# Kernel tuning notes

Measured on AMD Instinct MI355X. Metric: run time of the kernel, lower is better.

The kernel has to match this reference:

```python
import jax, jax.numpy as jnp
import numpy as np

TAU = 0.1          # contrastive_temperature
EPS = 0.05         # property_epsilon
L_LOCAL_G, L_GLOBAL, L_SC_G, L_LOCAL_SC, G_PROP = 1.0, 0.8, 1.0, 0.8, 0.5
B = 4096
D = 256
NUM_PROPS = 4
N_ATOMS = 131072
N_MOTIFS = 32768


def setup_inputs() -> dict:
    key = jax.random.key(0)
    ks = jax.random.split(key, 10)
    return {
        "emb_g_mole": jax.random.normal(ks[0], (B, D), jnp.float32),
        "emb_g_frag": jax.random.normal(ks[1], (N_ATOMS, D), jnp.float32),
        "emb_sc_mole": jax.random.normal(ks[2], (B, D), jnp.float32),
        "emb_sc_shape": jax.random.normal(ks[3], (N_MOTIFS, D), jnp.float32),
        "emb_motif": jax.random.normal(ks[4], (N_MOTIFS, D), jnp.float32),
        "emb_shape": jax.random.normal(ks[5], (N_MOTIFS, D), jnp.float32),
        # scaled so duplicate rows are the only pairs within EPS (realistic sparse mask)
        "prop_pred": jax.random.normal(ks[6], (B, NUM_PROPS), jnp.float32) * 0.05,
        "prop_target": jax.random.normal(ks[7], (B, NUM_PROPS), jnp.float32) * 0.05,
        "batch_g": jax.random.randint(ks[8], (N_ATOMS,), 0, B, jnp.int32),
        "batch_sc": jax.random.randint(ks[9], (N_MOTIFS,), 0, B, jnp.int32),
    }


def _contrastive(emb, props):
    # SupervisedContrastiveLoss: normalized cosine logits, mask from sqrt(cdist) < eps
    n = emb.shape[0]
    e = emb / jnp.maximum(jnp.linalg.norm(emb, axis=1, keepdims=True), 1e-12)
    logits = jnp.matmul(e, e.T) / TAU                       # [n, n]
    log_probs = jax.nn.log_softmax(logits, axis=1)
    sq = jnp.sum(props * props, axis=1)
    d2 = jnp.maximum(sq[:, None] + sq[None, :] - 2.0 * jnp.matmul(props, props.T), 0.0)
    dd = jnp.sqrt(jnp.sqrt(d2)) + 1e-8                      # cdist(...).sqrt() + 1e-8
    mask = (dd < EPS) & (~jnp.eye(n, dtype=bool))           # fill_diagonal_(0)
    cnt = jnp.sum(mask, axis=1)
    row_loss = -jnp.sum(jnp.where(mask, log_probs, 0.0), axis=1) / jnp.maximum(cnt, 1)
    valid = cnt > 0
    nvalid = jnp.sum(valid)
    loss = jnp.sum(jnp.where(valid, row_loss, 0.0)) / jnp.maximum(nvalid, 1)
    return jnp.where(nvalid > 0, loss, 0.0)


def _frag_alignment(emb_g_frag, emb_motif, batch_g, batch_sc):
    ones_g = jnp.ones((emb_g_frag.shape[0],), emb_g_frag.dtype)
    ones_s = jnp.ones((emb_motif.shape[0],), emb_motif.dtype)
    cnt_g = jax.ops.segment_sum(ones_g, batch_g, num_segments=B)
    cnt_s = jax.ops.segment_sum(ones_s, batch_sc, num_segments=B)
    mean_g = jax.ops.segment_sum(emb_g_frag, batch_g, num_segments=B) / jnp.maximum(cnt_g, 1.0)[:, None]
    mean_s = jax.ops.segment_sum(emb_motif, batch_sc, num_segments=B) / jnp.maximum(cnt_s, 1.0)[:, None]
    norms = jnp.linalg.norm(mean_g - mean_s, axis=1)
    valid = (cnt_g > 0) & (cnt_s > 0)
    batch_size = batch_g.max().astype(emb_g_frag.dtype) + 1.0
    return jnp.sum(jnp.where(valid, norms, 0.0)) / batch_size


def reference(emb_g_mole, emb_g_frag, emb_sc_mole, emb_sc_shape, emb_motif,
              emb_shape, prop_pred, prop_target, batch_g, batch_sc):
    l_local_g = _frag_alignment(emb_g_frag, emb_motif, batch_g, batch_sc)
    combined_emb = jnp.concatenate([emb_g_mole, emb_sc_mole], axis=0)    # [2B, d]
    combined_props = jnp.concatenate([prop_pred, prop_pred], axis=0)      # [2B, p]
    l_contr = _contrastive(combined_emb, combined_props)
    l_global = l_contr          # same inputs in both calls -> identical value
    l_local_sc = l_contr
    l_sc_g = jnp.mean(jnp.linalg.norm(emb_sc_shape - emb_shape, axis=1))  # AlignmentLoss mean
    l_prop = jnp.mean((prop_pred - prop_target) ** 2)                     # MSELoss
    l_hes = (L_LOCAL_G * l_local_g + L_GLOBAL * l_global + L_SC_G * l_sc_g
             + L_LOCAL_SC * l_local_sc + G_PROP * l_prop)
    # stacked: [l_hes, l_local_g, l_global, l_sc_g, l_local_sc, l_prop]
    return jnp.stack([l_hes, l_local_g, l_global, l_sc_g, l_local_sc, l_prop])
```

## Files before the change

kernel.cpp:

```cpp
#include <hip/hip_runtime.h>
#include <hip/hip_bf16.h>
#include <stdint.h>

typedef unsigned short u16;
typedef float f32x4 __attribute__((ext_vector_type(4)));
typedef short s16x8 __attribute__((ext_vector_type(8)));
typedef u16   u16x8 __attribute__((ext_vector_type(8)));
typedef u16   u16x4 __attribute__((ext_vector_type(4)));
typedef uint32_t u32x4 __attribute__((ext_vector_type(4)));

#define B_      4096
#define D_      256
#define NA_     131072
#define NM_     32768
#define N2_     8192
#define THR4    6.2499950e-6f
#define K2E     14.426950408889634f

#define OFF_CNT_G   0u
#define OFF_CNT_S   16384u
#define OFF_CUR_G   32768u
#define OFF_CUR_S   49152u
#define OFF_NB      65536u
#define OFF_SCAL    81920u
#define OFF_S       98304u
#define ZERO_BYTES  131072u
#define OFF_T       131072u
#define OFF_C       163840u
#define OFF_PLIST   196608u
#define OFF_OFFS_G  720896u
#define OFF_OFFS_S  737280u
#define OFF_SORT_G  753664u
#define OFF_SORT_S  1277952u
#define OFF_E       1409024u
#define WS_NEED     5603328u

__device__ inline float wave_sum(float v) {
#pragma unroll
  for (int m = 1; m < 64; m <<= 1) v += __shfl_xor(v, m, 64);
  return v;
}
__device__ inline int wave_sum_i(int v) {
#pragma unroll
  for (int m = 1; m < 64; m <<= 1) v += __shfl_xor(v, m, 64);
  return v;
}
__device__ inline u16 f2bf(float f) {
  uint32_t u = __float_as_uint(f);
  uint32_t r = (u + 0x7FFFu + ((u >> 16) & 1u)) >> 16;
  return (u16)r;
}
__device__ inline float bf2f(u16 v) { return __uint_as_float(((uint32_t)v) << 16); }

__device__ inline void gload16(const u16* __restrict__ g, u16* l) {
  __builtin_amdgcn_global_load_lds(
      (const __attribute__((address_space(1))) uint32_t*)g,
      (__attribute__((address_space(3))) uint32_t*)l, 16, 0, 0);
}

__global__ void k_zero(u32x4* __restrict__ p) {
  u32x4 z = {0u, 0u, 0u, 0u};
  p[blockIdx.x * 256 + threadIdx.x] = z;
}

__global__ void k_count(const int* __restrict__ bg, const int* __restrict__ bs,
                        int* cntg, int* cnts, int* bmax) {
  int i = blockIdx.x * 256 + threadIdx.x;
  int b = -1;
  if (i < NA_) { b = bg[i]; atomicAdd(&cntg[b], 1); }
  if (i < NM_) { atomicAdd(&cnts[bs[i]], 1); }
  int m = b;
#pragma unroll
  for (int k = 1; k < 64; k <<= 1) m = max(m, __shfl_xor(m, k, 64));
  if ((threadIdx.x & 63) == 0 && m >= 0) atomicMax(bmax, m);
}

__global__ void k_scan(const int* __restrict__ cntg, const int* __restrict__ cnts,
                       int* offsg, int* offss, int* curg, int* curs) {
  const int* cnt = blockIdx.x == 0 ? cntg : cnts;
  int* offs = blockIdx.x == 0 ? offsg : offss;
  int* cur  = blockIdx.x == 0 ? curg  : curs;
  __shared__ int ls[256];
  int t = threadIdx.x;
  int v[16]; int s = 0;
#pragma unroll
  for (int k = 0; k < 16; k++) { v[k] = cnt[t * 16 + k]; s += v[k]; }
  ls[t] = s;
  __syncthreads();
  for (int off = 1; off < 256; off <<= 1) {
    int add = (t >= off) ? ls[t - off] : 0;
    __syncthreads();
    ls[t] += add;
    __syncthreads();
  }
  int pre = t ? ls[t - 1] : 0;
#pragma unroll
  for (int k = 0; k < 16; k++) { offs[t * 16 + k] = pre; cur[t * 16 + k] = pre; pre += v[k]; }
}

__device__ inline void wave_row_sum(const float* __restrict__ src,
                                    const int* __restrict__ sorted,
                                    int off, int cnt, int lane, f32x4* accs) {
  f32x4 a0 = {0.f,0.f,0.f,0.f}, a1 = a0, a2 = a0, a3 = a0;
  f32x4 a4 = a0, a5 = a0, a6 = a0, a7 = a0;
  for (int base = 0; base < cnt; base += 64) {
    int n = min(cnt - base, 64);
    int idx = (lane < n) ? sorted[off + base + lane] : 0;
    int k = 0;
    for (; k + 7 < n; k += 8) {
      int i0 = __shfl(idx, k,     64), i1 = __shfl(idx, k + 1, 64);
      int i2 = __shfl(idx, k + 2, 64), i3 = __shfl(idx, k + 3, 64);
      int i4 = __shfl(idx, k + 4, 64), i5 = __shfl(idx, k + 5, 64);
      int i6 = __shfl(idx, k + 6, 64), i7 = __shfl(idx, k + 7, 64);
      a0 += *(const f32x4*)(src + (size_t)i0 * D_ + lane * 4);
      a1 += *(const f32x4*)(src + (size_t)i1 * D_ + lane * 4);
      a2 += *(const f32x4*)(src + (size_t)i2 * D_ + lane * 4);
      a3 += *(const f32x4*)(src + (size_t)i3 * D_ + lane * 4);
      a4 += *(const f32x4*)(src + (size_t)i4 * D_ + lane * 4);
      a5 += *(const f32x4*)(src + (size_t)i5 * D_ + lane * 4);
      a6 += *(const f32x4*)(src + (size_t)i6 * D_ + lane * 4);
      a7 += *(const f32x4*)(src + (size_t)i7 * D_ + lane * 4);
    }
    for (; k < n; k++) {
      int i0 = __shfl(idx, k, 64);
      a0 += *(const f32x4*)(src + (size_t)i0 * D_ + lane * 4);
    }
  }
  *accs = ((a0 + a1) + (a2 + a3)) + ((a4 + a5) + (a6 + a7));
}

__global__ __launch_bounds__(256) void k_fuseA(
    const int* __restrict__ bg, const int* __restrict__ bs,
    int* __restrict__ curg, int* __restrict__ curs,
    int* __restrict__ sortg, int* __restrict__ sorts,
    const float* __restrict__ gm, const float* __restrict__ scm,
    const float* __restrict__ scs, const float* __restrict__ shp,
    const float* __restrict__ pp,
    u16* __restrict__ E, int* __restrict__ nb, int* __restrict__ plist,
    float* __restrict__ scal) {
  int t = threadIdx.x, w = t >> 6, lane = t & 63;
  int blk = blockIdx.x;

  if (blk < 4096) {
    int a = blk;
    f32x4 pa = *(const f32x4*)(pp + (size_t)a * 4);
    for (int b = t; b < B_; b += 256) {
      f32x4 pb = *(const f32x4*)(pp + (size_t)b * 4);
      float dx = pa.x - pb.x, dy = pa.y - pb.y, dz = pa.z - pb.z, dw = pa.w - pb.w;
      float d2 = dx * dx + dy * dy + dz * dz + dw * dw;
      if (d2 < THR4) {
        int pos = atomicAdd(&nb[a], 1);
        if (pos < 32) plist[a * 32 + pos] = b;
      }
    }
  } else if (blk < 4608) {
    int i = (blk - 4096) * 256 + t;
    if (i < NA_) { int b = bg[i]; sortg[atomicAdd(&curg[b], 1)] = i; }
    if (i < NM_) { int b = bs[i]; sorts[atomicAdd(&curs[b], 1)] = i; }
  } else if (blk < 6656) {
    int r = (blk - 4608) * 4 + w;
    const float* src = (r < B_) ? gm + (size_t)r * D_ : scm + (size_t)(r - B_) * D_;
    f32x4 v = *(const f32x4*)(src + lane * 4);
    float ss = v.x * v.x + v.y * v.y + v.z * v.z + v.w * v.w;
    ss = wave_sum(ss);
    float inv = 1.f / fmaxf(sqrtf(ss), 1e-12f);
    u16x4 o;
    o.x = f2bf(v.x * inv); o.y = f2bf(v.y * inv);
    o.z = f2bf(v.z * inv); o.w = f2bf(v.w * inv);
    *(u16x4*)(E + (size_t)r * D_ + lane * 4) = o;
  } else {
    int wg = (blk - 6656) * 4 + w;
    float acc = 0.f;
    for (int r = wg; r < NM_; r += 8192) {
      f32x4 va = *(const f32x4*)(scs + (size_t)r * D_ + lane * 4);
      f32x4 vb = *(const f32x4*)(shp + (size_t)r * D_ + lane * 4);
      float dx = va.x - vb.x, dy = va.y - vb.y, dz = va.z - vb.z, dw = va.w - vb.w;
      float ss = wave_sum(dx * dx + dy * dy + dz * dz + dw * dw);
      if (lane == 0) acc += sqrtf(ss);
    }
    __shared__ float sr4[4];
    if (lane == 0) sr4[w] = acc;
    __syncthreads();
    if (t == 0) atomicAdd(&scal[1], sr4[0] + sr4[1] + sr4[2] + sr4[3]);
  }
}

__global__ __launch_bounds__(256) void k_fuseB(
    const u16* __restrict__ E,
    const float* __restrict__ fg, const float* __restrict__ fm,
    const int* __restrict__ cntg, const int* __restrict__ cnts,
    const int* __restrict__ offsg, const int* __restrict__ offss,
    const int* __restrict__ sortg, const int* __restrict__ sorts,
    const int* __restrict__ nb, const int* __restrict__ plist,
    float* __restrict__ S, float* __restrict__ T, int* __restrict__ C,
    float* __restrict__ scal) {
  __shared__ __align__(16) u16 As[128 * 64];
  __shared__ __align__(16) u16 Bs[128 * 64];
  int blk = blockIdx.x;
  int tid = threadIdx.x, lane = tid & 63, wid = tid >> 6;

  if (blk < 1024) {
    int b = blk * 4 + wid;
    int cg = cntg[b], cs = cnts[b];
    int og = offsg[b], os = offss[b];
    f32x4 sg, ss;
    wave_row_sum(fg, sortg, og, cg, lane, &sg);
    wave_row_sum(fm, sorts, os, cs, lane, &ss);
    float ig = 1.f / fmaxf((float)cg, 1.f);
    float is = 1.f / fmaxf((float)cs, 1.f);
    float dx = sg.x * ig - ss.x * is, dy = sg.y * ig - ss.y * is;
    float dz = sg.z * ig - ss.z * is, dw = sg.w * ig - ss.w * is;
    float v = wave_sum(dx * dx + dy * dy + dz * dz + dw * dw);
    __shared__ float r2[4];
    if (lane == 0) r2[wid] = (cg > 0 && cs > 0) ? sqrtf(v) : 0.f;
    __syncthreads();
    if (tid == 0) {
      float s = r2[0] + r2[1] + r2[2] + r2[3];
      if (s != 0.f) atomicAdd(&scal[0], s);
    }
    return;
  }

  if (blk >= 3104) {
    int i = (blk - 3104) * 4 + wid;
    int a = i & (B_ - 1);
    int n = min(nb[a], 32);
    u16x4 vi = *(const u16x4*)(E + (size_t)i * D_ + lane * 4);
    float ex = bf2f(vi.x), ey = bf2f(vi.y), ez = bf2f(vi.z), ew = bf2f(vi.w);
    float acc = -(ex * ex + ey * ey + ez * ez + ew * ew);
    for (int k = 0; k < n; k++) {
      int b = plist[a * 32 + k];
      u16x4 v1 = *(const u16x4*)(E + (size_t)b * D_ + lane * 4);
      u16x4 v2 = *(const u16x4*)(E + (size_t)(b + B_) * D_ + lane * 4);
      acc += ex * bf2f(v1.x) + ey * bf2f(v1.y) + ez * bf2f(v1.z) + ew * bf2f(v1.w);
      acc += ex * bf2f(v2.x) + ey * bf2f(v2.y) + ez * bf2f(v2.z) + ew * bf2f(v2.w);
    }
    acc = wave_sum(acc);
    if (lane == 0) { T[i] = 10.0f * acc; C[i] = 2 * n - 1; }
    return;
  }

  int t = blk - 1024;
  int bi = (int)((129.0f - sqrtf(129.0f * 129.0f - 8.0f * (float)t)) * 0.5f);
  while ((bi + 1) * (129 - (bi + 1)) / 2 <= t) bi++;
  while (bi * (129 - bi) / 2 > t) bi--;
  int bj = bi + (t - bi * (129 - bi) / 2);

  int row0 = bi * 128, col0 = bj * 128;
  int wr = wid >> 1, wc = wid & 1;

  int rsub = lane >> 3;
  int csw  = (((lane & 7) ^ rsub) << 4) >> 1;

  f32x4 acc[4][4];
#pragma unroll
  for (int mi = 0; mi < 4; mi++)
#pragma unroll
    for (int ni = 0; ni < 4; ni++) {
      f32x4 z = {0.f, 0.f, 0.f, 0.f};
      acc[mi][ni] = z;
    }

  for (int kc = 0; kc < 4; ++kc) {
    __syncthreads();
#pragma unroll
    for (int it = 0; it < 4; it++) {
      int s = wid * 4 + it;
      int r = s * 8 + rsub;
      gload16(E + (size_t)(row0 + r) * D_ + kc * 64 + csw, As + s * 512);
      gload16(E + (size_t)(col0 + r) * D_ + kc * 64 + csw, Bs + s * 512);
    }
    __syncthreads();
#pragma unroll
    for (int kk = 0; kk < 2; ++kk) {
      s16x8 af[4], bfr[4];
#pragma unroll
      for (int mi = 0; mi < 4; mi++) {
        int rA = wr * 64 + mi * 16 + (lane & 15);
        int cbf = kk * 64 + (lane >> 4) * 16;
        int addr = rA * 128 + (cbf ^ ((rA & 7) << 4));
        af[mi] = *(const s16x8*)((const char*)As + addr);
      }
#pragma unroll
      for (int ni = 0; ni < 4; ni++) {
        int rB = wc * 64 + ni * 16 + (lane & 15);
        int cbf = kk * 64 + (lane >> 4) * 16;
        int addr = rB * 128 + (cbf ^ ((rB & 7) << 4));
        bfr[ni] = *(const s16x8*)((const char*)Bs + addr);
      }
#pragma unroll
      for (int mi = 0; mi < 4; mi++)
#pragma unroll
        for (int ni = 0; ni < 4; ni++)
          acc[mi][ni] = __builtin_amdgcn_mfma_f32_16x16x32_bf16(af[mi], bfr[ni], acc[mi][ni], 0, 0, 0);
    }
  }

  int g = lane >> 4, cl = lane & 15;
  float colsum[4] = {0.f, 0.f, 0.f, 0.f};
#pragma unroll
  for (int mi = 0; mi < 4; mi++) {
#pragma unroll
    for (int reg = 0; reg < 4; ++reg) {
      int gi = row0 + wr * 64 + mi * 16 + g * 4 + reg;
      float vs = 0.f;
#pragma unroll
      for (int ni = 0; ni < 4; ni++) {
        float e = exp2f(acc[mi][ni][reg] * K2E - K2E);
        vs += e;
        colsum[ni] += e;
      }
#pragma unroll
      for (int m = 1; m < 16; m <<= 1) vs += __shfl_xor(vs, m, 64);
      if (cl == 0) atomicAdd(&S[gi], vs);
    }
  }
  if (bi != bj) {
#pragma unroll
    for (int ni = 0; ni < 4; ni++) {
      float cs = colsum[ni];
      cs += __shfl_xor(cs, 16, 64);
      cs += __shfl_xor(cs, 32, 64);
      if (g == 0) atomicAdd(&S[col0 + wc * 64 + ni * 16 + cl], cs);
    }
  }
}

__global__ void k_final(const float* __restrict__ S, const float* __restrict__ T,
                        const int* __restrict__ C, const float* __restrict__ scal,
                        const float* __restrict__ pp, const float* __restrict__ pt,
                        float* __restrict__ out) {
  float sp = 0.f;
  for (int i = threadIdx.x; i < B_ * 4; i += 256) {
    float d = pp[i] - pt[i];
    sp += d * d;
  }
  float rls = 0.f; int nv = 0;
  for (int i = threadIdx.x; i < N2_; i += 256) {
    int ci = C[i];
    if (ci > 0) { rls += (10.0f + logf(S[i])) - T[i] / (float)ci; nv++; }
  }
  rls = wave_sum(rls);
  sp  = wave_sum(sp);
  nv  = wave_sum_i(nv);
  __shared__ float r1[4], r3[4]; __shared__ int r2[4];
  int lane = threadIdx.x & 63, w = threadIdx.x >> 6;
  if (lane == 0) { r1[w] = rls; r2[w] = nv; r3[w] = sp; }
  __syncthreads();
  if (threadIdx.x == 0) {
    float rtot = r1[0] + r1[1] + r1[2] + r1[3];
    int nvt = r2[0] + r2[1] + r2[2] + r2[3];
    float sptot = r3[0] + r3[1] + r3[2] + r3[3];
    float l_contr = nvt > 0 ? rtot / (float)nvt : 0.f;
    int bmax = ((const int*)scal)[3];
    float bs = (float)bmax + 1.0f;
    float l_local_g = scal[0] / bs;
    float l_sc = scal[1] / (float)NM_;
    float l_prop = sptot / (float)(B_ * 4);
    float l_hes = 1.0f * l_local_g + 0.8f * l_contr + 1.0f * l_sc + 0.8f * l_contr + 0.5f * l_prop;
    out[0] = l_hes; out[1] = l_local_g; out[2] = l_contr;
    out[3] = l_sc;  out[4] = l_contr;   out[5] = l_prop;
  }
}

extern "C" void kernel_launch(void* const* d_in, const int* in_sizes, int n_in,
                              void* d_out, int out_size, void* d_ws, size_t ws_size,
                              hipStream_t stream) {
  if (ws_size < WS_NEED) return;
  const float* gm  = (const float*)d_in[0];
  const float* fg  = (const float*)d_in[1];
  const float* scm = (const float*)d_in[2];
  const float* scs = (const float*)d_in[3];
  const float* mot = (const float*)d_in[4];
  const float* shp = (const float*)d_in[5];
  const float* pp  = (const float*)d_in[6];
  const float* pt  = (const float*)d_in[7];
  const int* bg = (const int*)d_in[8];
  const int* bs = (const int*)d_in[9];
  float* out = (float*)d_out;
  char* ws = (char*)d_ws;

  int* cntg  = (int*)(ws + OFF_CNT_G);
  int* cnts  = (int*)(ws + OFF_CNT_S);
  int* curg  = (int*)(ws + OFF_CUR_G);
  int* curs  = (int*)(ws + OFF_CUR_S);
  int* nb    = (int*)(ws + OFF_NB);
  float* scal = (float*)(ws + OFF_SCAL);
  float* S   = (float*)(ws + OFF_S);
  float* T   = (float*)(ws + OFF_T);
  int* C     = (int*)(ws + OFF_C);
  int* plist = (int*)(ws + OFF_PLIST);
  int* offsg = (int*)(ws + OFF_OFFS_G);
  int* offss = (int*)(ws + OFF_OFFS_S);
  int* sortg = (int*)(ws + OFF_SORT_G);
  int* sorts = (int*)(ws + OFF_SORT_S);
  u16* E     = (u16*)(ws + OFF_E);

  k_zero<<<32, 256, 0, stream>>>((u32x4*)ws);
  k_count<<<512, 256, 0, stream>>>(bg, bs, cntg, cnts, (int*)scal + 3);
  k_scan<<<2, 256, 0, stream>>>(cntg, cnts, offsg, offss, curg, curs);
  k_fuseA<<<8704, 256, 0, stream>>>(bg, bs, curg, curs, sortg, sorts,
                                    gm, scm, scs, shp, pp, E, nb, plist, scal);
  k_fuseB<<<5152, 256, 0, stream>>>(E, fg, mot, cntg, cnts, offsg, offss,
                                    sortg, sorts, nb, plist, S, T, C, scal);
  k_final<<<1, 256, 0, stream>>>(S, T, C, scal, pp, pt, out);
}
```

Baseline: 213.4 us.

## Restructure stage fusion and interleave segment, GEMM and diag blocks in fuseB

Moves the histogram count into the fused elementwise kernel and splits the scatter into its own small kernel after the scan. In k_fuseB, segment-sum, GEMM-tile and diagonal-term blocks are interleaved by a proportional index mapping instead of being laid out in contiguous ranges. The diagonal-term blocks now each handle 32 rows, cutting the grid from 5152 to 3360 blocks. The aim is to balance memory-bound and compute-bound blocks across the GPU and shorten tail effects, at the cost of an extra kernel launch and more index arithmetic.

```diff
diff --git a/kernel.cpp b/kernel.cpp
--- a/kernel.cpp
+++ b/kernel.cpp
@@ -16,6 +16,12 @@
 #define N2_     8192
 #define THR4    6.2499950e-6f
 #define K2E     14.426950408889634f
+
+#define NS_   1024
+#define NG_   2080
+#define NT_   256
+#define NTOT_ 3360
+#define NR_   2336
 
 #define OFF_CNT_G   0u
 #define OFF_CNT_S   16384u
@@ -63,16 +69,64 @@
   p[blockIdx.x * 256 + threadIdx.x] = z;
 }
 
-__global__ void k_count(const int* __restrict__ bg, const int* __restrict__ bs,
-                        int* cntg, int* cnts, int* bmax) {
-  int i = blockIdx.x * 256 + threadIdx.x;
-  int b = -1;
-  if (i < NA_) { b = bg[i]; atomicAdd(&cntg[b], 1); }
-  if (i < NM_) { atomicAdd(&cnts[bs[i]], 1); }
-  int m = b;
-#pragma unroll
-  for (int k = 1; k < 64; k <<= 1) m = max(m, __shfl_xor(m, k, 64));
-  if ((threadIdx.x & 63) == 0 && m >= 0) atomicMax(bmax, m);
+__global__ __launch_bounds__(256) void k_fuseA(
+    const int* __restrict__ bg, const int* __restrict__ bs,
+    int* __restrict__ cntg, int* __restrict__ cnts, int* __restrict__ bmax,
+    const float* __restrict__ gm, const float* __restrict__ scm,
+    const float* __restrict__ scs, const float* __restrict__ shp,
+    const float* __restrict__ pp,
+    u16* __restrict__ E, int* __restrict__ nb, int* __restrict__ plist,
+    float* __restrict__ scal) {
+  int t = threadIdx.x, w = t >> 6, lane = t & 63;
+  int blk = blockIdx.x;
+
+  if (blk < 512) {
+    int i = blk * 256 + t;
+    int b = -1;
+    if (i < NA_) { b = bg[i]; atomicAdd(&cntg[b], 1); }
+    if (i < NM_) { atomicAdd(&cnts[bs[i]], 1); }
+    int m = b;
+#pragma unroll
+    for (int k = 1; k < 64; k <<= 1) m = max(m, __shfl_xor(m, k, 64));
+    if ((t & 63) == 0 && m >= 0) atomicMax(bmax, m);
+  } else if (blk < 4608) {
+    int a = blk - 512;
+    f32x4 pa = *(const f32x4*)(pp + (size_t)a * 4);
+    for (int b = t; b < B_; b += 256) {
+      f32x4 pb = *(const f32x4*)(pp + (size_t)b * 4);
+      float dx = pa.x - pb.x, dy = pa.y - pb.y, dz = pa.z - pb.z, dw = pa.w - pb.w;
+      float d2 = dx * dx + dy * dy + dz * dz + dw * dw;
+      if (d2 < THR4) {
+        int pos = atomicAdd(&nb[a], 1);
+        if (pos < 32) plist[a * 32 + pos] = b;
+      }
+    }
+  } else if (blk < 6656) {
+    int r = (blk - 4608) * 4 + w;
+    const float* src = (r < B_) ? gm + (size_t)r * D_ : scm + (size_t)(r - B_) * D_;
+    f32x4 v = *(const f32x4*)(src + lane * 4);
+    float ss = v.x * v.x + v.y * v.y + v.z * v.z + v.w * v.w;
+    ss = wave_sum(ss);
+    float inv = 1.f / fmaxf(sqrtf(ss), 1e-12f);
+    u16x4 o;
+    o.x = f2bf(v.x * inv); o.y = f2bf(v.y * inv);
+    o.z = f2bf(v.z * inv); o.w = f2bf(v.w * inv);
+    *(u16x4*)(E + (size_t)r * D_ + lane * 4) = o;
+  } else {
+    int wg = (blk - 6656) * 4 + w;
+    float acc = 0.f;
+    for (int r = wg; r < NM_; r += 8192) {
+      f32x4 va = *(const f32x4*)(scs + (size_t)r * D_ + lane * 4);
+      f32x4 vb = *(const f32x4*)(shp + (size_t)r * D_ + lane * 4);
+      float dx = va.x - vb.x, dy = va.y - vb.y, dz = va.z - vb.z, dw = va.w - vb.w;
+      float ss = wave_sum(dx * dx + dy * dy + dz * dz + dw * dw);
+      if (lane == 0) acc += sqrtf(ss);
+    }
+    __shared__ float sr4[4];
+    if (lane == 0) sr4[w] = acc;
+    __syncthreads();
+    if (t == 0) atomicAdd(&scal[1], sr4[0] + sr4[1] + sr4[2] + sr4[3]);
+  }
 }
 
 __global__ void k_scan(const int* __restrict__ cntg, const int* __restrict__ cnts,
@@ -96,6 +150,13 @@
   int pre = t ? ls[t - 1] : 0;
 #pragma unroll
   for (int k = 0; k < 16; k++) { offs[t * 16 + k] = pre; cur[t * 16 + k] = pre; pre += v[k]; }
+}
+
+__global__ void k_scatter(const int* __restrict__ bg, const int* __restrict__ bs,
+                          int* curg, int* curs, int* sortg, int* sorts) {
+  int i = blockIdx.x * 256 + threadIdx.x;
+  if (i < NA_) { int b = bg[i]; sortg[atomicAdd(&curg[b], 1)] = i; }
+  if (i < NM_) { int b = bs[i]; sorts[atomicAdd(&curs[b], 1)] = i; }
 }
 
 __device__ inline void wave_row_sum(const float* __restrict__ src,
@@ -129,62 +190,6 @@
   *accs = ((a0 + a1) + (a2 + a3)) + ((a4 + a5) + (a6 + a7));
 }
 
-__global__ __launch_bounds__(256) void k_fuseA(
-    const int* __restrict__ bg, const int* __restrict__ bs,
-    int* __restrict__ curg, int* __restrict__ curs,
-    int* __restrict__ sortg, int* __restrict__ sorts,
-    const float* __restrict__ gm, const float* __restrict__ scm,
-    const float* __restrict__ scs, const float* __restrict__ shp,
-    const float* __restrict__ pp,
-    u16* __restrict__ E, int* __restrict__ nb, int* __restrict__ plist,
-    float* __restrict__ scal) {
-  int t = threadIdx.x, w = t >> 6, lane = t & 63;
-  int blk = blockIdx.x;
-
-  if (blk < 4096) {
-    int a = blk;
-    f32x4 pa = *(const f32x4*)(pp + (size_t)a * 4);
-    for (int b = t; b < B_; b += 256) {
-      f32x4 pb = *(const f32x4*)(pp + (size_t)b * 4);
-      float dx = pa.x - pb.x, dy = pa.y - pb.y, dz = pa.z - pb.z, dw = pa.w - pb.w;
-      float d2 = dx * dx + dy * dy + dz * dz + dw * dw;
-      if (d2 < THR4) {
-        int pos = atomicAdd(&nb[a], 1);
-        if (pos < 32) plist[a * 32 + pos] = b;
-      }
-    }
-  } else if (blk < 4608) {
-    int i = (blk - 4096) * 256 + t;
-    if (i < NA_) { int b = bg[i]; sortg[atomicAdd(&curg[b], 1)] = i; }
-    if (i < NM_) { int b = bs[i]; sorts[atomicAdd(&curs[b], 1)] = i; }
-  } else if (blk < 6656) {
-    int r = (blk - 4608) * 4 + w;
-    const float* src = (r < B_) ? gm + (size_t)r * D_ : scm + (size_t)(r - B_) * D_;
-    f32x4 v = *(const f32x4*)(src + lane * 4);
-    float ss = v.x * v.x + v.y * v.y + v.z * v.z + v.w * v.w;
-    ss = wave_sum(ss);
-    float inv = 1.f / fmaxf(sqrtf(ss), 1e-12f);
-    u16x4 o;
-    o.x = f2bf(v.x * inv); o.y = f2bf(v.y * inv);
-    o.z = f2bf(v.z * inv); o.w = f2bf(v.w * inv);
-    *(u16x4*)(E + (size_t)r * D_ + lane * 4) = o;
-  } else {
-    int wg = (blk - 6656) * 4 + w;
-    float acc = 0.f;
-    for (int r = wg; r < NM_; r += 8192) {
-      f32x4 va = *(const f32x4*)(scs + (size_t)r * D_ + lane * 4);
-      f32x4 vb = *(const f32x4*)(shp + (size_t)r * D_ + lane * 4);
-      float dx = va.x - vb.x, dy = va.y - vb.y, dz = va.z - vb.z, dw = va.w - vb.w;
-      float ss = wave_sum(dx * dx + dy * dy + dz * dz + dw * dw);
-      if (lane == 0) acc += sqrtf(ss);
-    }
-    __shared__ float sr4[4];
-    if (lane == 0) sr4[w] = acc;
-    __syncthreads();
-    if (t == 0) atomicAdd(&scal[1], sr4[0] + sr4[1] + sr4[2] + sr4[3]);
-  }
-}
-
 __global__ __launch_bounds__(256) void k_fuseB(
     const u16* __restrict__ E,
     const float* __restrict__ fg, const float* __restrict__ fm,
@@ -199,8 +204,11 @@
   int blk = blockIdx.x;
   int tid = threadIdx.x, lane = tid & 63, wid = tid >> 6;
 
-  if (blk < 1024) {
-    int b = blk * 4 + wid;
+  int64_t p = (int64_t)blk * NS_;
+  int srem = (int)(p % NTOT_);
+  if (srem < NS_) {
+    int sid = (int)(p / NTOT_);
+    int b = sid * 4 + wid;
     int cg = cntg[b], cs = cnts[b];
     int og = offsg[b], os = offss[b];
     f32x4 sg, ss;
@@ -221,26 +229,34 @@
     return;
   }
 
-  if (blk >= 3104) {
-    int i = (blk - 3104) * 4 + wid;
-    int a = i & (B_ - 1);
-    int n = min(nb[a], 32);
-    u16x4 vi = *(const u16x4*)(E + (size_t)i * D_ + lane * 4);
-    float ex = bf2f(vi.x), ey = bf2f(vi.y), ez = bf2f(vi.z), ew = bf2f(vi.w);
-    float acc = -(ex * ex + ey * ey + ez * ez + ew * ew);
-    for (int k = 0; k < n; k++) {
-      int b = plist[a * 32 + k];
-      u16x4 v1 = *(const u16x4*)(E + (size_t)b * D_ + lane * 4);
-      u16x4 v2 = *(const u16x4*)(E + (size_t)(b + B_) * D_ + lane * 4);
-      acc += ex * bf2f(v1.x) + ey * bf2f(v1.y) + ez * bf2f(v1.z) + ew * bf2f(v1.w);
-      acc += ex * bf2f(v2.x) + ey * bf2f(v2.y) + ez * bf2f(v2.z) + ew * bf2f(v2.w);
-    }
-    acc = wave_sum(acc);
-    if (lane == 0) { T[i] = 10.0f * acc; C[i] = 2 * n - 1; }
+  int r = blk - (int)((p + NTOT_ - 1) / NTOT_);
+  int64_t q = (int64_t)r * NG_;
+  int grem = (int)(q % NR_);
+
+  if (grem >= NG_) {
+    int tix = r - (int)((q + NR_ - 1) / NR_);
+#pragma unroll
+    for (int k8 = 0; k8 < 8; k8++) {
+      int i = tix * 32 + wid * 8 + k8;
+      int a = i & (B_ - 1);
+      int n = min(nb[a], 32);
+      u16x4 vi = *(const u16x4*)(E + (size_t)i * D_ + lane * 4);
+      float ex = bf2f(vi.x), ey = bf2f(vi.y), ez = bf2f(vi.z), ew = bf2f(vi.w);
+      float acc = -(ex * ex + ey * ey + ez * ez + ew * ew);
+      for (int k = 0; k < n; k++) {
+        int b = plist[a * 32 + k];
+        u16x4 v1 = *(const u16x4*)(E + (size_t)b * D_ + lane * 4);
+        u16x4 v2 = *(const u16x4*)(E + (size_t)(b + B_) * D_ + lane * 4);
+        acc += ex * bf2f(v1.x) + ey * bf2f(v1.y) + ez * bf2f(v1.z) + ew * bf2f(v1.w);
+        acc += ex * bf2f(v2.x) + ey * bf2f(v2.y) + ez * bf2f(v2.z) + ew * bf2f(v2.w);
+      }
+      acc = wave_sum(acc);
+      if (lane == 0) { T[i] = 10.0f * acc; C[i] = 2 * n - 1; }
+    }
     return;
   }
 
-  int t = blk - 1024;
+  int t = (int)(q / NR_);
   int bi = (int)((129.0f - sqrtf(129.0f * 129.0f - 8.0f * (float)t)) * 0.5f);
   while ((bi + 1) * (129 - (bi + 1)) / 2 <= t) bi++;
   while (bi * (129 - bi) / 2 > t) bi--;
@@ -266,9 +282,9 @@
 #pragma unroll
     for (int it = 0; it < 4; it++) {
       int s = wid * 4 + it;
-      int r = s * 8 + rsub;
-      gload16(E + (size_t)(row0 + r) * D_ + kc * 64 + csw, As + s * 512);
-      gload16(E + (size_t)(col0 + r) * D_ + kc * 64 + csw, Bs + s * 512);
+      int rr = s * 8 + rsub;
+      gload16(E + (size_t)(row0 + rr) * D_ + kc * 64 + csw, As + s * 512);
+      gload16(E + (size_t)(col0 + rr) * D_ + kc * 64 + csw, Bs + s * 512);
     }
     __syncthreads();
 #pragma unroll
@@ -397,11 +413,11 @@
   u16* E     = (u16*)(ws + OFF_E);
 
   k_zero<<<32, 256, 0, stream>>>((u32x4*)ws);
-  k_count<<<512, 256, 0, stream>>>(bg, bs, cntg, cnts, (int*)scal + 3);
+  k_fuseA<<<8704, 256, 0, stream>>>(bg, bs, cntg, cnts, (int*)scal + 3,
+                                    gm, scm, scs, shp, pp, E, nb, plist, scal);
   k_scan<<<2, 256, 0, stream>>>(cntg, cnts, offsg, offss, curg, curs);
-  k_fuseA<<<8704, 256, 0, stream>>>(bg, bs, curg, curs, sortg, sorts,
-                                    gm, scm, scs, shp, pp, E, nb, plist, scal);
-  k_fuseB<<<5152, 256, 0, stream>>>(E, fg, mot, cntg, cnts, offsg, offss,
-                                    sortg, sorts, nb, plist, S, T, C, scal);
+  k_scatter<<<512, 256, 0, stream>>>(bg, bs, curg, curs, sortg, sorts);
+  k_fuseB<<<NTOT_, 256, 0, stream>>>(E, fg, mot, cntg, cnts, offsg, offss,
+                                     sortg, sorts, nb, plist, S, T, C, scal);
   k_final<<<1, 256, 0, stream>>>(S, T, C, scal, pp, pt, out);
 }
```

Measured after the change: 212.6 us. About the same (-0.4%).
